# Kernel tuning notes

Hardware: AMD Instinct MI355X
Metric: run time of the kernel (lower is better)

Reference implementation:

```python
import jax, jax.numpy as jnp
import numpy as np
import math
from jax import lax


def _conv(x, w, b=None):
    # NCHW conv, stride 1, SAME padding (matches k=3,p=1 and k=1,p=0)
    y = lax.conv_general_dilated(x, w, (1, 1), 'SAME',
                                 dimension_numbers=('NCHW', 'OIHW', 'NCHW'))
    if b is not None:
        y = y + b[None, :, None, None]
    return y


def _bn(x):
    # BatchNorm2d(affine=False) in training mode: batch statistics, eps=1e-5
    m = x.mean(axis=(0, 2, 3), keepdims=True)
    v = x.var(axis=(0, 2, 3), keepdims=True)
    return (x - m) * lax.rsqrt(v + 1e-5)


def _basic(x, w):
    # BasicLayer: Conv -> BN(affine=False) -> ReLU
    return jax.nn.relu(_bn(_conv(x, w)))


def _grid_sample(img, grid):
    # torch F.grid_sample, mode='bilinear', align_corners=False, zero padding
    # img: (B,C,H,W), grid: (B,Hg,Wg,2) in [-1,1] (x,y)
    B, C, H, W = img.shape
    x = (grid[..., 0] + 1.0) * (W * 0.5) - 0.5
    y = (grid[..., 1] + 1.0) * (H * 0.5) - 0.5
    x0 = jnp.floor(x)
    y0 = jnp.floor(y)
    wx = x - x0
    wy = y - y0
    x0i = x0.astype(jnp.int32)
    y0i = y0.astype(jnp.int32)

    def samp(im, yi, xi):
        valid = ((xi >= 0) & (xi < W) & (yi >= 0) & (yi < H)).astype(im.dtype)
        v = im[:, jnp.clip(yi, 0, H - 1), jnp.clip(xi, 0, W - 1)]  # (C,Hg,Wg)
        return v * valid[None]

    def per_b(im, y0i, x0i, wx, wy):
        v00 = samp(im, y0i, x0i)
        v01 = samp(im, y0i, x0i + 1)
        v10 = samp(im, y0i + 1, x0i)
        v11 = samp(im, y0i + 1, x0i + 1)
        return (v00 * (1 - wx) * (1 - wy) + v01 * wx * (1 - wy)
                + v10 * (1 - wx) * wy + v11 * wx * wy)

    return jax.vmap(per_b)(img, y0i, x0i, wx, wy)


def _pos_grid(H, W, dtype):
    # meshgrid(indexing='xy'), stacked (x,y), reshaped row-major over (H,W)
    xs = jnp.linspace(-1 + 1.0 / W, 1 - 1.0 / W, W, dtype=dtype)
    ys = jnp.linspace(-1 + 1.0 / H, 1 - 1.0 / H, H, dtype=dtype)
    gx, gy = jnp.meshgrid(xs, ys, indexing='xy')  # (H,W)
    return jnp.stack([gx, gy], axis=-1).reshape(H * W, 2)


def setup_inputs() -> dict:
    key = jax.random.key(0)
    ks = jax.random.split(key, 16)
    B, Cc, Hc, Wc = 4, 64, 64, 64
    Cf, Hf, Wf = 24, 128, 128

    def w(k, shape):
        fan_in = shape[1] * shape[2] * shape[3]
        return jax.random.normal(k, shape, jnp.float32) / np.sqrt(fan_in).astype(np.float32)

    return {
        'feats0_c': jax.random.normal(ks[0], (B, Cc, Hc, Wc), jnp.float32),
        'feats1_c': jax.random.normal(ks[1], (B, Cc, Hc, Wc), jnp.float32),
        'feats0_f': jax.random.normal(ks[2], (B, Cf, Hf, Wf), jnp.float32),
        'feats1_f': jax.random.normal(ks[3], (B, Cf, Hf, Wf), jnp.float32),
        'cw1': w(ks[4], (256, 130, 3, 3)),
        'cw2': w(ks[5], (256, 256, 3, 3)),
        'cw3': w(ks[6], (256, 256, 3, 3)),
        'cw4': w(ks[7], (256, 256, 3, 3)),
        'cw5': w(ks[8], (3, 256, 1, 1)),
        'cb5': jax.random.normal(ks[9], (3,), jnp.float32) * 0.01,
        'fw1': w(ks[10], (64, 50, 3, 3)),
        'fw2': w(ks[11], (64, 64, 3, 3)),
        'fw3': w(ks[12], (64, 64, 3, 3)),
        'fw4': w(ks[13], (64, 64, 3, 3)),
        'fw5': w(ks[14], (3, 64, 1, 1)),
        'fb5': jax.random.normal(ks[15], (3,), jnp.float32) * 0.01,
    }


def reference(feats0_c, feats1_c, feats0_f, feats1_f,
              cw1, cw2, cw3, cw4, cw5, cb5,
              fw1, fw2, fw3, fw4, fw5, fb5):
    B, C, Hc, Wc = feats0_c.shape
    # corr_volume: einsum('bci,bcj->bji') -> (B, HW_1, Hc, Wc) over feat0 positions
    corr = jnp.einsum('bchw,bcj->bjhw', feats0_c,
                      feats1_c.reshape(B, C, Hc * Wc)) / math.sqrt(C)
    # pos_embed: softmax over feat1 positions, expected grid position
    P = jax.nn.softmax(corr, axis=1)
    g = _pos_grid(Hc, Wc, corr.dtype)  # (HW, 2)
    coarse_warp = jnp.einsum('bjhw,jd->bdhw', P, g)  # (B,2,Hc,Wc)
    coarse_matches0 = jnp.concatenate(
        [coarse_warp, jnp.zeros_like(coarse_warp[:, -1:])], axis=1)  # (B,3,Hc,Wc)

    warped1c = _grid_sample(feats1_c,
                            jnp.moveaxis(coarse_matches0, 1, -1)[..., :2])
    x = jnp.concatenate([feats0_c, warped1c, coarse_warp], axis=1)  # 130 ch
    for w_ in (cw1, cw2, cw3, cw4):
        x = _basic(x, w_)
    coarse_matches = coarse_matches0 + _conv(x, cw5, cb5)

    Hf, Wf = feats0_f.shape[-2:]
    up = jax.image.resize(coarse_matches, (B, 3, Hf, Wf), method='bilinear')
    up_d = lax.stop_gradient(up)  # torch .detach()
    warped1f = _grid_sample(feats1_f, jnp.moveaxis(up_d, 1, -1)[..., :2])
    y = jnp.concatenate([feats0_f, warped1f, up_d[:, :2]], axis=1)  # 50 ch
    for w_ in (fw1, fw2, fw3, fw4):
        y = _basic(y, w_)
    fine_matches = up_d + _conv(y, fw5, fb5)

    # corresps[8]['flow'/'certainty'] and corresps[4]['flow'/'certainty']
    return coarse_matches, fine_matches
```

## Files before the change

kernel.cpp:

```cpp
#include <hip/hip_runtime.h>
#include <hip/hip_bf16.h>

using bf16 = __hip_bfloat16;
typedef unsigned short ushort_t;
typedef __attribute__((ext_vector_type(8))) short v8s;
typedef __attribute__((ext_vector_type(4))) float v4f;

__device__ __forceinline__ float bfbits2f(unsigned u) {
    return __uint_as_float(u << 16);
}
__device__ __forceinline__ ushort_t f2bfbits(float f) {
    unsigned x = __float_as_uint(f);
    return (ushort_t)((x + 0x7fffu + ((x >> 16) & 1u)) >> 16);
}
__device__ __forceinline__ float ldin(const void* p, size_t i, int f32) {
    return f32 ? ((const float*)p)[i] : bfbits2f(((const ushort_t*)p)[i]);
}
__device__ __forceinline__ void stout(void* p, size_t i, float v, int f32) {
    if (f32) ((float*)p)[i] = v;
    else     ((ushort_t*)p)[i] = f2bfbits(v);
}

#define B_   4
#define CC   64
#define HC   64
#define WC   64
#define JC   4096
#define CF   24
#define HF   128
#define WF   128
#define JF   16384
#define OUT0_ELEMS (B_ * 3 * JC)

__global__ void dtype_probe_kernel(const ushort_t* __restrict__ x,
                                   int* __restrict__ flag)
{
    __shared__ int cnt;
    if (threadIdx.x == 0) cnt = 0;
    __syncthreads();
    int c = 0;
    for (int i = threadIdx.x; i < 8192; i += 256) {
        const unsigned e = (x[i] >> 7) & 0xFF;
        if (e >= 0x89) ++c;
    }
    atomicAdd(&cnt, c);
    __syncthreads();
    if (threadIdx.x == 0) *flag = (cnt > 64) ? 1 : 0;
}

__global__ void repack_w_kernel(const void* __restrict__ w, ushort_t* __restrict__ wp,
                                int CO, int CIreal, int CIP, const int* __restrict__ dflag)
{
    const int f32 = *dflag;
    const int idx = blockIdx.x * 256 + threadIdx.x;
    const int total = 9 * CO * CIP;
    if (idx >= total) return;
    const int k = idx / (CO * CIP);
    const int rem = idx - k * (CO * CIP);
    const int co = rem / CIP;
    const int cip = rem - co * CIP;
    float v = 0.f;
    if (cip < CIreal) v = ldin(w, ((size_t)co * CIreal + cip) * 9 + k, f32);
    wp[((size_t)k * CO + co) * CIP + cip] = f2bfbits(v);
}

__global__ void repack_wfrag_kernel(const void* __restrict__ w, ushort_t* __restrict__ wfrag,
                                    int CIreal, int nch, const int* __restrict__ dflag)
{
    const int f32 = *dflag;
    const int idx = blockIdx.x * 256 + threadIdx.x;
    const int total = 8 * 9 * 2 * 2 * nch * 64;
    if (idx >= total) return;
    const int ln = idx & 63;
    int t = idx >> 6;
    const int ch = t % nch; t /= nch;
    const int pl = t & 1; t >>= 1;
    const int nt = t & 1; t >>= 1;
    const int k = t % 9;
    const int cog = t / 9;
    const int co = cog * 32 + nt * 16 + (ln & 15);
    const int cib = ch * 32 + (ln >> 4) * 8;
    ushort_t vals[8];
#pragma unroll
    for (int e = 0; e < 8; ++e) {
        const int ci = cib + e;
        float v = 0.f;
        if (ci < CIreal) v = ldin(w, ((size_t)co * CIreal + ci) * 9 + k, f32);
        const ushort_t h = f2bfbits(v);
        vals[e] = pl ? f2bfbits(v - bfbits2f(h)) : h;
    }
    uint4 o;
    o.x = (unsigned)vals[0] | ((unsigned)vals[1] << 16);
    o.y = (unsigned)vals[2] | ((unsigned)vals[3] << 16);
    o.z = (unsigned)vals[4] | ((unsigned)vals[5] << 16);
    o.w = (unsigned)vals[6] | ((unsigned)vals[7] << 16);
    *(uint4*)&wfrag[(size_t)idx * 8] = o;
}

__global__ __launch_bounds__(256) void split_transpose_kernel(
    const void* __restrict__ src, ushort_t* __restrict__ hi,
    ushort_t* __restrict__ lo, const int* __restrict__ dflag)
{
    const int f32 = *dflag;
    __shared__ float t[64][65];
    const int blk = blockIdx.x;
    const int b = blk >> 6;
    const int px0 = (blk & 63) * 64;
    const int tid = threadIdx.x;
    const int px = tid & 63;
    for (int i = 0; i < 16; ++i) {
        const int c = (tid >> 6) + 4 * i;
        t[px][c] = ldin(src, ((size_t)b * 64 + c) * 4096 + px0 + px, f32);
    }
    __syncthreads();
    for (int it = 0; it < 2; ++it) {
        const int p = tid + it * 256;
        const int opx = p >> 3, chk = (p & 7) * 8;
        unsigned hh[4], ll[4];
#pragma unroll
        for (int e = 0; e < 4; ++e) {
            const float v0 = t[opx][chk + 2 * e];
            const float v1 = t[opx][chk + 2 * e + 1];
            const ushort_t h0 = f2bfbits(v0);
            const ushort_t h1 = f2bfbits(v1);
            hh[e] = (unsigned)h0 | ((unsigned)h1 << 16);
            ll[e] = (unsigned)f2bfbits(v0 - bfbits2f(h0))
                  | ((unsigned)f2bfbits(v1 - bfbits2f(h1)) << 16);
        }
        const size_t obase = ((size_t)b * 4096 + px0 + opx) * 64 + chk;
        *(uint4*)&hi[obase] = make_uint4(hh[0], hh[1], hh[2], hh[3]);
        *(uint4*)&lo[obase] = make_uint4(ll[0], ll[1], ll[2], ll[3]);
    }
}

#define KCH 128
__global__ __launch_bounds__(256) void corr_mfma_kernel(
    const ushort_t* __restrict__ qhi, const ushort_t* __restrict__ qlo,
    const ushort_t* __restrict__ khi, const ushort_t* __restrict__ klo,
    float* __restrict__ part)
{
    __shared__ ushort_t kbh[KCH * 72];
    __shared__ ushort_t kbl[KCH * 72];
    __shared__ float red[4][64][3];
    const int h = blockIdx.x, b = blockIdx.y, sl = blockIdx.z;
    const int tid = threadIdx.x;
    const int wv = tid >> 6, ln = tid & 63;
    const int lm = ln & 15, quad = ln >> 4, q8 = quad * 8;

    v8s qf[4][2][2];
#pragma unroll
    for (int mt = 0; mt < 4; ++mt)
#pragma unroll
        for (int kc = 0; kc < 2; ++kc) {
            const size_t qoff = ((size_t)b * 4096 + h * 64 + mt * 16 + lm) * 64 + kc * 32 + q8;
            qf[mt][kc][0] = *(const v8s*)&qhi[qoff];
            qf[mt][kc][1] = *(const v8s*)&qlo[qoff];
        }

    float P[4][4][3];
#pragma unroll
    for (int mt = 0; mt < 4; ++mt)
#pragma unroll
        for (int i = 0; i < 4; ++i)
            P[mt][i][0] = P[mt][i][1] = P[mt][i][2] = 0.f;

    const size_t kbase = (size_t)b * 4096 * 64;
    for (int c = 0; c < 1024 / KCH; ++c) {
        const int j0 = sl * 1024 + c * KCH;
        __syncthreads();
        for (int p = tid; p < 2048; p += 256) {
            const int pl = p >> 10;
            const int r = p & 1023;
            const int key = r >> 3, chk = (r & 7) * 8;
            const ushort_t* gsrc = pl ? klo : khi;
            const uint4 v = *(const uint4*)&gsrc[kbase + (size_t)(j0 + key) * 64 + chk];
            ushort_t* dst = pl ? kbl : kbh;
            *(uint4*)&dst[key * 72 + chk] = v;
        }
        __syncthreads();

#pragma unroll
        for (int nt = 0; nt < 2; ++nt) {
            const int kb = wv * 32 + nt * 16;
            const int j = j0 + kb + lm;
            const float gx = (float)((j & 63) * 2 + 1) * (1.f / 64.f) - 1.f;
            const float gy = (float)((j >> 6) * 2 + 1) * (1.f / 64.f) - 1.f;
            const v8s bh0 = *(const v8s*)&kbh[(kb + lm) * 72 + q8];
            const v8s bh1 = *(const v8s*)&kbh[(kb + lm) * 72 + 32 + q8];
            const v8s bl0 = *(const v8s*)&kbl[(kb + lm) * 72 + q8];
            const v8s bl1 = *(const v8s*)&kbl[(kb + lm) * 72 + 32 + q8];
#pragma unroll
            for (int mt = 0; mt < 4; ++mt) {
                v4f acc = (v4f)(0.f);
                acc = __builtin_amdgcn_mfma_f32_16x16x32_bf16(qf[mt][0][0], bl0, acc, 0, 0, 0);
                acc = __builtin_amdgcn_mfma_f32_16x16x32_bf16(qf[mt][0][1], bh0, acc, 0, 0, 0);
                acc = __builtin_amdgcn_mfma_f32_16x16x32_bf16(qf[mt][0][0], bh0, acc, 0, 0, 0);
                acc = __builtin_amdgcn_mfma_f32_16x16x32_bf16(qf[mt][1][0], bl1, acc, 0, 0, 0);
                acc = __builtin_amdgcn_mfma_f32_16x16x32_bf16(qf[mt][1][1], bh1, acc, 0, 0, 0);
                acc = __builtin_amdgcn_mfma_f32_16x16x32_bf16(qf[mt][1][0], bh1, acc, 0, 0, 0);
#pragma unroll
                for (int i = 0; i < 4; ++i) {
                    const float p_ = __expf(acc[i] * 0.125f);
                    P[mt][i][0] += p_;
                    P[mt][i][1] += p_ * gx;
                    P[mt][i][2] += p_ * gy;
                }
            }
        }
    }

#pragma unroll
    for (int mt = 0; mt < 4; ++mt)
#pragma unroll
        for (int i = 0; i < 4; ++i)
#pragma unroll
            for (int d = 0; d < 3; ++d) {
                float v = P[mt][i][d];
                v += __shfl_xor(v, 1);
                v += __shfl_xor(v, 2);
                v += __shfl_xor(v, 4);
                v += __shfl_xor(v, 8);
                P[mt][i][d] = v;
            }
    if (lm == 0) {
#pragma unroll
        for (int mt = 0; mt < 4; ++mt)
#pragma unroll
            for (int i = 0; i < 4; ++i) {
                const int q = mt * 16 + quad * 4 + i;
                red[wv][q][0] = P[mt][i][0];
                red[wv][q][1] = P[mt][i][1];
                red[wv][q][2] = P[mt][i][2];
            }
    }
    __syncthreads();
    if (tid < 64) {
        const int q = tid;
        float l = 0.f, ax = 0.f, ay = 0.f;
        for (int w = 0; w < 4; ++w) {
            l += red[w][q][0]; ax += red[w][q][1]; ay += red[w][q][2];
        }
        const size_t base = (((size_t)sl * B_ + b) * 4096 + h * 64 + q) * 4;
        part[base] = l; part[base + 1] = ax; part[base + 2] = ay;
    }
}

__global__ __launch_bounds__(256) void corr_reduce_kernel(
    const float* __restrict__ part, float* __restrict__ cm0)
{
    const int idx = blockIdx.x * 256 + threadIdx.x;
    const int b = idx >> 12, hq = idx & 4095;
    float l = 0.f, ax = 0.f, ay = 0.f;
    for (int s = 0; s < 4; ++s) {
        const size_t base = (((size_t)s * B_ + b) * 4096 + hq) * 4;
        l += part[base]; ax += part[base + 1]; ay += part[base + 2];
    }
    const float inv = 1.f / l;
    const size_t o = (size_t)b * 3 * JC + hq;
    cm0[o]          = ax * inv;
    cm0[o + JC]     = ay * inv;
    cm0[o + 2 * JC] = 0.f;
}

__global__ __launch_bounds__(256) void coarse_concat_split(
    const void* __restrict__ f0c, const void* __restrict__ f1c,
    const float* __restrict__ cm0, ushort_t* __restrict__ hiP,
    ushort_t* __restrict__ loP, const int* __restrict__ dflag)
{
    const int f32 = *dflag;
    const int idx = blockIdx.x * 256 + threadIdx.x;
    const int b = idx >> 12, hw = idx & (JC - 1);
    const size_t ib = (size_t)b * CC * JC;
    ushort_t* oh = hiP + (size_t)idx * 160;
    ushort_t* ol = loP + (size_t)idx * 160;

#pragma unroll 4
    for (int c = 0; c < CC; ++c) {
        const float v = ldin(f0c, ib + (size_t)c * JC + hw, f32);
        const ushort_t h = f2bfbits(v);
        oh[c] = h; ol[c] = f2bfbits(v - bfbits2f(h));
    }

    const float gx = cm0[((size_t)b * 3 + 0) * JC + hw];
    const float gy = cm0[((size_t)b * 3 + 1) * JC + hw];
    const float x = (gx + 1.f) * 32.f - 0.5f;
    const float y = (gy + 1.f) * 32.f - 0.5f;
    const float x0f = floorf(x), y0f = floorf(y);
    const float wx = x - x0f, wy = y - y0f;
    const int x0 = (int)x0f, y0 = (int)y0f;
    const int x1 = x0 + 1, y1 = y0 + 1;
    const float vx0 = (x0 >= 0 && x0 < WC) ? 1.f : 0.f;
    const float vx1 = (x1 >= 0 && x1 < WC) ? 1.f : 0.f;
    const float vy0 = (y0 >= 0 && y0 < HC) ? 1.f : 0.f;
    const float vy1 = (y1 >= 0 && y1 < HC) ? 1.f : 0.f;
    const int cx0 = min(max(x0, 0), WC - 1), cx1 = min(max(x1, 0), WC - 1);
    const int cy0 = min(max(y0, 0), HC - 1), cy1 = min(max(y1, 0), HC - 1);
    const float w00 = (1.f - wx) * (1.f - wy) * vx0 * vy0;
    const float w01 = wx * (1.f - wy) * vx1 * vy0;
    const float w10 = (1.f - wx) * wy * vx0 * vy1;
    const float w11 = wx * wy * vx1 * vy1;
    const int i00 = cy0 * WC + cx0, i01 = cy0 * WC + cx1;
    const int i10 = cy1 * WC + cx0, i11 = cy1 * WC + cx1;

#pragma unroll 4
    for (int c = 0; c < CC; ++c) {
        const size_t pb = ib + (size_t)c * JC;
        const float v = w00 * ldin(f1c, pb + i00, f32) + w01 * ldin(f1c, pb + i01, f32)
                      + w10 * ldin(f1c, pb + i10, f32) + w11 * ldin(f1c, pb + i11, f32);
        const ushort_t h = f2bfbits(v);
        oh[64 + c] = h; ol[64 + c] = f2bfbits(v - bfbits2f(h));
    }
    {
        const ushort_t h = f2bfbits(gx);
        oh[128] = h; ol[128] = f2bfbits(gx - bfbits2f(h));
    }
    {
        const ushort_t h = f2bfbits(gy);
        oh[129] = h; ol[129] = f2bfbits(gy - bfbits2f(h));
    }
    for (int c = 130; c < 160; ++c) { oh[c] = 0; ol[c] = 0; }
}

__global__ __launch_bounds__(256) void bnrelu_split_kernel(
    const float* __restrict__ x, const float2* __restrict__ st,
    ushort_t* __restrict__ hiP, ushort_t* __restrict__ loP)
{
    const int idx = blockIdx.x * 256 + threadIdx.x;
    const int px = idx >> 5;
    const int c8 = (idx & 31) << 3;
    const float4 v0 = *(const float4*)&x[(size_t)px * 256 + c8];
    const float4 v1 = *(const float4*)&x[(size_t)px * 256 + c8 + 4];
    const float vv[8] = {v0.x, v0.y, v0.z, v0.w, v1.x, v1.y, v1.z, v1.w};
    ushort_t hh[8], ll[8];
#pragma unroll
    for (int e = 0; e < 8; ++e) {
        const float2 s = st[c8 + e];
        const float f = fmaxf((vv[e] - s.x) * s.y, 0.f);
        const ushort_t h = f2bfbits(f);
        hh[e] = h; ll[e] = f2bfbits(f - bfbits2f(h));
    }
    uint4 oh, ol;
    oh.x = (unsigned)hh[0] | ((unsigned)hh[1] << 16);
    oh.y = (unsigned)hh[2] | ((unsigned)hh[3] << 16);
    oh.z = (unsigned)hh[4] | ((unsigned)hh[5] << 16);
    oh.w = (unsigned)hh[6] | ((unsigned)hh[7] << 16);
    ol.x = (unsigned)ll[0] | ((unsigned)ll[1] << 16);
    ol.y = (unsigned)ll[2] | ((unsigned)ll[3] << 16);
    ol.z = (unsigned)ll[4] | ((unsigned)ll[5] << 16);
    ol.w = (unsigned)ll[6] | ((unsigned)ll[7] << 16);
    *(uint4*)&hiP[(size_t)px * 256 + c8] = oh;
    *(uint4*)&loP[(size_t)px * 256 + c8] = ol;
}

__global__ __launch_bounds__(256, 3) void conv3x3_wsplit(
    const ushort_t* __restrict__ hiP, const ushort_t* __restrict__ loP,
    const ushort_t* __restrict__ wfrag,
    float* __restrict__ out, float* __restrict__ chsum,
    int CIP, int CO, int H, int W, int tilesX)
{
    __shared__ ushort_t actH[18 * 18 * 36];
    __shared__ ushort_t actL[18 * 18 * 36];
    __shared__ float smS[4][2][16], smQ[4][2][16];

    const int nch = CIP >> 5;
    const int tid = threadIdx.x;
    const int tile = blockIdx.x;
    const int b = blockIdx.y;
    const int cog = blockIdx.z;
    const int ty = (tile / tilesX) * 16;
    const int tx = (tile % tilesX) * 16;
    const int wv = tid >> 6;
    const int ln = tid & 63;
    const int lm = ln & 15;
    const int q8 = (ln >> 4) * 8;

    v4f acc[4][2];
#pragma unroll
    for (int i = 0; i < 4; ++i)
#pragma unroll
        for (int j = 0; j < 2; ++j) acc[i][j] = (v4f)(0.f);

    for (int ch = 0; ch < nch; ++ch) {
        const int ci0 = ch << 5;
        __syncthreads();
        for (int p = tid; p < 2592; p += 256) {
            const int pl = (p >= 1296) ? 1 : 0;
            const int r = p - pl * 1296;
            const int yy = r / 72;
            const int rem = r - yy * 72;
            const int xx = rem >> 2;
            const int cs = (rem & 3) << 3;
            const int gy = ty + yy - 1, gx = tx + xx - 1;
            uint4 val = make_uint4(0u, 0u, 0u, 0u);
            if (gy >= 0 && gy < H && gx >= 0 && gx < W) {
                const ushort_t* src = pl ? loP : hiP;
                val = *(const uint4*)&src[(((size_t)(b * H + gy)) * W + gx) * CIP + ci0 + cs];
            }
            ushort_t* dst = pl ? actL : actH;
            *(uint4*)&dst[(yy * 18 + xx) * 36 + cs] = val;
        }
        __syncthreads();

#pragma unroll
        for (int dx = 0; dx < 3; ++dx) {
            v8s ah[6], al[6];
#pragma unroll
            for (int rr = 0; rr < 6; ++rr) {
                const int aoff = ((wv * 4 + rr) * 18 + lm + dx) * 36 + q8;
                ah[rr] = *(const v8s*)&actH[aoff];
                al[rr] = *(const v8s*)&actL[aoff];
            }
#pragma unroll
            for (int dy = 0; dy < 3; ++dy) {
                const int k = dy * 3 + dx;
                const size_t fb = (((size_t)(cog * 9 + k) * 4) * nch + ch) * 64 + ln;
                const size_t step = (size_t)nch * 64;
                const v8s bh0 = *(const v8s*)&wfrag[fb * 8];
                const v8s bl0 = *(const v8s*)&wfrag[(fb + step) * 8];
                const v8s bh1 = *(const v8s*)&wfrag[(fb + 2 * step) * 8];
                const v8s bl1 = *(const v8s*)&wfrag[(fb + 3 * step) * 8];
#pragma unroll
                for (int mt = 0; mt < 4; ++mt) {
                    const v8s a_h = ah[mt + dy];
                    const v8s a_l = al[mt + dy];
                    acc[mt][0] = __builtin_amdgcn_mfma_f32_16x16x32_bf16(a_h, bl0, acc[mt][0], 0, 0, 0);
                    acc[mt][0] = __builtin_amdgcn_mfma_f32_16x16x32_bf16(a_l, bh0, acc[mt][0], 0, 0, 0);
                    acc[mt][0] = __builtin_amdgcn_mfma_f32_16x16x32_bf16(a_h, bh0, acc[mt][0], 0, 0, 0);
                    acc[mt][1] = __builtin_amdgcn_mfma_f32_16x16x32_bf16(a_h, bl1, acc[mt][1], 0, 0, 0);
                    acc[mt][1] = __builtin_amdgcn_mfma_f32_16x16x32_bf16(a_l, bh1, acc[mt][1], 0, 0, 0);
                    acc[mt][1] = __builtin_amdgcn_mfma_f32_16x16x32_bf16(a_h, bh1, acc[mt][1], 0, 0, 0);
                }
            }
        }
    }

#pragma unroll
    for (int mt = 0; mt < 4; ++mt) {
        const int y = ty + wv * 4 + mt;
#pragma unroll
        for (int nt = 0; nt < 2; ++nt) {
            const int co = cog * 32 + nt * 16 + lm;
#pragma unroll
            for (int i = 0; i < 4; ++i) {
                const int x = tx + ((ln >> 4) << 2) + i;
                out[(((size_t)(b * H + y)) * W + x) * CO + co] = acc[mt][nt][i];
            }
        }
    }

    float s0 = 0.f, s1 = 0.f, q0 = 0.f, q1 = 0.f;
#pragma unroll
    for (int mt = 0; mt < 4; ++mt)
#pragma unroll
        for (int i = 0; i < 4; ++i) {
            float v = acc[mt][0][i]; s0 += v; q0 += v * v;
            v = acc[mt][1][i]; s1 += v; q1 += v * v;
        }
    s0 += __shfl_xor(s0, 16); s0 += __shfl_xor(s0, 32);
    s1 += __shfl_xor(s1, 16); s1 += __shfl_xor(s1, 32);
    q0 += __shfl_xor(q0, 16); q0 += __shfl_xor(q0, 32);
    q1 += __shfl_xor(q1, 16); q1 += __shfl_xor(q1, 32);
    __syncthreads();
    if (ln < 16) {
        smS[wv][0][ln] = s0; smS[wv][1][ln] = s1;
        smQ[wv][0][ln] = q0; smQ[wv][1][ln] = q1;
    }
    __syncthreads();
    if (tid < 32) {
        const int nt = tid >> 4, l2 = tid & 15;
        float S = 0.f, Q = 0.f;
        for (int w = 0; w < 4; ++w) { S += smS[w][nt][l2]; Q += smQ[w][nt][l2]; }
        const int co = cog * 32 + nt * 16 + l2;
        atomicAdd(&chsum[2 * co], S);
        atomicAdd(&chsum[2 * co + 1], Q);
    }
}

template <bool BN>
__global__ __launch_bounds__(256) void conv3x3_mfma(
    const ushort_t* __restrict__ in,
    const ushort_t* __restrict__ wp,
    const float2* __restrict__ stats,
    ushort_t* __restrict__ out, float* __restrict__ chsum,
    int CI, int CO, int H, int W, int tilesX)
{
    __shared__ ushort_t act[18 * 18 * 40];
    __shared__ ushort_t wbuf[9 * 32 * 40];
    __shared__ float2 st[256];
    __shared__ float smS[4][2][16], smQ[4][2][16];

    const int tid = threadIdx.x;
    const int tile = blockIdx.x;
    const int b = blockIdx.y;
    const int cog = blockIdx.z;
    const int ty = (tile / tilesX) * 16;
    const int tx = (tile % tilesX) * 16;
    const int wv = tid >> 6;
    const int ln = tid & 63;
    const int lm = ln & 15;
    const int q8 = (ln >> 4) * 8;

    if (BN) for (int c = tid; c < CI; c += 256) st[c] = stats[c];

    v4f acc[4][2];
#pragma unroll
    for (int i = 0; i < 4; ++i)
#pragma unroll
        for (int j = 0; j < 2; ++j) acc[i][j] = (v4f)(0.f);

    const int nChunks = CI >> 5;
    for (int ch = 0; ch < nChunks; ++ch) {
        const int ci0 = ch << 5;
        __syncthreads();
        for (int p = tid; p < 1296; p += 256) {
            const int yy = p / 72;
            const int rem = p - yy * 72;
            const int xx = rem >> 2;
            const int cs = (rem & 3) << 3;
            const int gy = ty + yy - 1, gx = tx + xx - 1;
            uint4 val = make_uint4(0u, 0u, 0u, 0u);
            if (gy >= 0 && gy < H && gx >= 0 && gx < W) {
                const ushort_t* gp = in + (((size_t)(b * H + gy)) * W + gx) * CI + ci0 + cs;
                val = *(const uint4*)gp;
                if (BN) {
                    unsigned u[4] = {val.x, val.y, val.z, val.w};
                    unsigned o[4];
#pragma unroll
                    for (int e = 0; e < 4; ++e) {
                        float lo = bfbits2f(u[e] & 0xffffu);
                        float hi = bfbits2f(u[e] >> 16);
                        const float2 s0 = st[ci0 + cs + 2 * e];
                        const float2 s1 = st[ci0 + cs + 2 * e + 1];
                        lo = fmaxf((lo - s0.x) * s0.y, 0.f);
                        hi = fmaxf((hi - s1.x) * s1.y, 0.f);
                        o[e] = (unsigned)f2bfbits(lo) | ((unsigned)f2bfbits(hi) << 16);
                    }
                    val = make_uint4(o[0], o[1], o[2], o[3]);
                }
            }
            *(uint4*)&act[(yy * 18 + xx) * 40 + cs] = val;
        }
        for (int p = tid; p < 1152; p += 256) {
            const int k = p / 128;
            const int rem = p - k * 128;
            const int co = rem >> 2;
            const int cs = (rem & 3) << 3;
            const ushort_t* gp = wp + ((size_t)k * CO + cog * 32 + co) * CI + ci0 + cs;
            *(uint4*)&wbuf[(k * 32 + co) * 40 + cs] = *(const uint4*)gp;
        }
        __syncthreads();

#pragma unroll
        for (int dx = 0; dx < 3; ++dx) {
            v8s af[6];
#pragma unroll
            for (int rr = 0; rr < 6; ++rr)
                af[rr] = *(const v8s*)&act[((wv * 4 + rr) * 18 + lm + dx) * 40 + q8];
#pragma unroll
            for (int dy = 0; dy < 3; ++dy) {
                const int k = dy * 3 + dx;
                const v8s bf0 = *(const v8s*)&wbuf[(k * 32 + lm) * 40 + q8];
                const v8s bf1 = *(const v8s*)&wbuf[(k * 32 + 16 + lm) * 40 + q8];
#pragma unroll
                for (int mt = 0; mt < 4; ++mt) {
                    acc[mt][0] = __builtin_amdgcn_mfma_f32_16x16x32_bf16(af[mt + dy], bf0, acc[mt][0], 0, 0, 0);
                    acc[mt][1] = __builtin_amdgcn_mfma_f32_16x16x32_bf16(af[mt + dy], bf1, acc[mt][1], 0, 0, 0);
                }
            }
        }
    }

#pragma unroll
    for (int mt = 0; mt < 4; ++mt) {
        const int y = ty + wv * 4 + mt;
#pragma unroll
        for (int nt = 0; nt < 2; ++nt) {
            const int co = cog * 32 + nt * 16 + lm;
#pragma unroll
            for (int i = 0; i < 4; ++i) {
                const int x = tx + ((ln >> 4) << 2) + i;
                out[(((size_t)(b * H + y)) * W + x) * CO + co] = f2bfbits(acc[mt][nt][i]);
            }
        }
    }

    float s0 = 0.f, s1 = 0.f, q0 = 0.f, q1 = 0.f;
#pragma unroll
    for (int mt = 0; mt < 4; ++mt)
#pragma unroll
        for (int i = 0; i < 4; ++i) {
            float v = acc[mt][0][i]; s0 += v; q0 += v * v;
            v = acc[mt][1][i]; s1 += v; q1 += v * v;
        }
    s0 += __shfl_xor(s0, 16); s0 += __shfl_xor(s0, 32);
    s1 += __shfl_xor(s1, 16); s1 += __shfl_xor(s1, 32);
    q0 += __shfl_xor(q0, 16); q0 += __shfl_xor(q0, 32);
    q1 += __shfl_xor(q1, 16); q1 += __shfl_xor(q1, 32);
    __syncthreads();
    if (ln < 16) {
        smS[wv][0][ln] = s0; smS[wv][1][ln] = s1;
        smQ[wv][0][ln] = q0; smQ[wv][1][ln] = q1;
    }
    __syncthreads();
    if (tid < 32) {
        const int nt = tid >> 4, l2 = tid & 15;
        float S = 0.f, Q = 0.f;
        for (int w = 0; w < 4; ++w) { S += smS[w][nt][l2]; Q += smQ[w][nt][l2]; }
        const int co = cog * 32 + nt * 16 + l2;
        atomicAdd(&chsum[2 * co], S);
        atomicAdd(&chsum[2 * co + 1], Q);
    }
}

__global__ void stats_finalize_kernel(const float* __restrict__ chsum,
                                      float2* __restrict__ st, int C, float inv_n)
{
    const int c = threadIdx.x;
    if (c >= C) return;
    const float mean = chsum[2 * c] * inv_n;
    const float var = chsum[2 * c + 1] * inv_n - mean * mean;
    st[c] = make_float2(mean, 1.0f / sqrtf(var + 1e-5f));
}

__global__ __launch_bounds__(256) void coarse_head_kernel(
    const float* __restrict__ A, const float2* __restrict__ stats,
    const void* __restrict__ w5, const void* __restrict__ b5,
    float* __restrict__ cm0, void* __restrict__ out,
    const int* __restrict__ dflag)
{
    const int f32 = *dflag;
    __shared__ float wl[3][256];
    __shared__ float bl[3];
    __shared__ float2 st[256];
    const int tid = threadIdx.x;
    for (int i = tid; i < 768; i += 256) wl[i >> 8][i & 255] = ldin(w5, i, f32);
    if (tid < 3) bl[tid] = ldin(b5, tid, f32);
    st[tid] = stats[tid];
    __syncthreads();

    const int idx = blockIdx.x * 256 + tid;
    const int b = idx >> 12, hw = idx & (JC - 1);
    float a0 = bl[0], a1 = bl[1], a2 = bl[2];
    const float* p = A + (size_t)idx * 256;
    for (int c = 0; c < 256; c += 4) {
        const float4 raw = *(const float4*)(p + c);
        const float rv[4] = {raw.x, raw.y, raw.z, raw.w};
#pragma unroll
        for (int e = 0; e < 4; ++e) {
            const int cc = c + e;
            const float v = fmaxf((rv[e] - st[cc].x) * st[cc].y, 0.f);
            a0 += v * wl[0][cc]; a1 += v * wl[1][cc]; a2 += v * wl[2][cc];
        }
    }
    const size_t base = (size_t)b * 3 * JC + hw;
    const float c0 = cm0[base] + a0;
    const float c1 = cm0[base + JC] + a1;
    const float c2 = cm0[base + 2 * JC] + a2;
    cm0[base] = c0; cm0[base + JC] = c1; cm0[base + 2 * JC] = c2;
    stout(out, base, c0, f32);
    stout(out, base + JC, c1, f32);
    stout(out, base + 2 * JC, c2, f32);
}

__global__ __launch_bounds__(256) void upsample_kernel(
    const float* __restrict__ cm, float* __restrict__ up)
{
    const int idx = blockIdx.x * 256 + threadIdx.x;
    const int ox = idx & 127, oy = (idx >> 7) & 127, bc = idx >> 14;
    const float sx = ox * 0.5f - 0.25f;
    const float sy = oy * 0.5f - 0.25f;
    const int x0 = (int)floorf(sx), y0 = (int)floorf(sy);
    const float fx = sx - x0, fy = sy - y0;
    const int cx0 = max(x0, 0), cx1 = min(x0 + 1, WC - 1);
    const int cy0 = max(y0, 0), cy1 = min(y0 + 1, HC - 1);
    const float* p = cm + (size_t)bc * JC;
    const float v = (1.f - fy) * ((1.f - fx) * p[cy0 * WC + cx0] + fx * p[cy0 * WC + cx1])
                  + fy * ((1.f - fx) * p[cy1 * WC + cx0] + fx * p[cy1 * WC + cx1]);
    up[idx] = v;
}

__global__ __launch_bounds__(256) void fine_concat_nhwc(
    const void* __restrict__ f0f, const void* __restrict__ f1f,
    const float* __restrict__ up, ushort_t* __restrict__ A,
    const int* __restrict__ dflag)
{
    const int f32 = *dflag;
    const int idx = blockIdx.x * 256 + threadIdx.x;
    const int b = idx >> 14, hw = idx & (JF - 1);
    const size_t ib = (size_t)b * CF * JF;
    ushort_t* o = A + (size_t)idx * 64;

    for (int c = 0; c < CF; ++c)
        o[c] = f2bfbits(ldin(f0f, ib + (size_t)c * JF + hw, f32));

    const size_t ub = (size_t)b * 3 * JF + hw;
    const float gx = up[ub], gy = up[ub + JF];
    const float x = (gx + 1.f) * 64.f - 0.5f;
    const float y = (gy + 1.f) * 64.f - 0.5f;
    const float x0f = floorf(x), y0f = floorf(y);
    const float wx = x - x0f, wy = y - y0f;
    const int x0 = (int)x0f, y0 = (int)y0f;
    const int x1 = x0 + 1, y1 = y0 + 1;
    const float vx0 = (x0 >= 0 && x0 < WF) ? 1.f : 0.f;
    const float vx1 = (x1 >= 0 && x1 < WF) ? 1.f : 0.f;
    const float vy0 = (y0 >= 0 && y0 < HF) ? 1.f : 0.f;
    const float vy1 = (y1 >= 0 && y1 < HF) ? 1.f : 0.f;
    const int cx0 = min(max(x0, 0), WF - 1), cx1 = min(max(x1, 0), WF - 1);
    const int cy0 = min(max(y0, 0), HF - 1), cy1 = min(max(y1, 0), HF - 1);
    const float w00 = (1.f - wx) * (1.f - wy) * vx0 * vy0;
    const float w01 = wx * (1.f - wy) * vx1 * vy0;
    const float w10 = (1.f - wx) * wy * vx0 * vy1;
    const float w11 = wx * wy * vx1 * vy1;
    const int i00 = cy0 * WF + cx0, i01 = cy0 * WF + cx1;
    const int i10 = cy1 * WF + cx0, i11 = cy1 * WF + cx1;

    for (int c = 0; c < CF; ++c) {
        const size_t pb = ib + (size_t)c * JF;
        const float v = w00 * ldin(f1f, pb + i00, f32) + w01 * ldin(f1f, pb + i01, f32)
                      + w10 * ldin(f1f, pb + i10, f32) + w11 * ldin(f1f, pb + i11, f32);
        o[24 + c] = f2bfbits(v);
    }
    o[48] = f2bfbits(gx);
    o[49] = f2bfbits(gy);
    for (int c = 50; c < 64; ++c) o[c] = 0;
}

__global__ __launch_bounds__(256) void fine_head_kernel(
    const ushort_t* __restrict__ A, const float2* __restrict__ stats,
    const void* __restrict__ w5, const void* __restrict__ b5,
    const float* __restrict__ up, void* __restrict__ out,
    const int* __restrict__ dflag)
{
    const int f32 = *dflag;
    __shared__ float wl[3][64];
    __shared__ float bl[3];
    __shared__ float2 st[64];
    const int tid = threadIdx.x;
    if (tid < 192) wl[tid >> 6][tid & 63] = ldin(w5, tid, f32);
    if (tid < 3) bl[tid] = ldin(b5, tid, f32);
    if (tid < 64) st[tid] = stats[tid];
    __syncthreads();

    const int idx = blockIdx.x * 256 + tid;
    const int b = idx >> 14, hw = idx & (JF - 1);
    float a0 = bl[0], a1 = bl[1], a2 = bl[2];
    const ushort_t* p = A + (size_t)idx * 64;
    for (int c = 0; c < 64; c += 8) {
        const uint4 raw = *(const uint4*)(p + c);
        const unsigned u[4] = {raw.x, raw.y, raw.z, raw.w};
#pragma unroll
        for (int e = 0; e < 4; ++e) {
            const int c0 = c + 2 * e, c1 = c0 + 1;
            float lo = bfbits2f(u[e] & 0xffffu);
            float hi = bfbits2f(u[e] >> 16);
            lo = fmaxf((lo - st[c0].x) * st[c0].y, 0.f);
            hi = fmaxf((hi - st[c1].x) * st[c1].y, 0.f);
            a0 += lo * wl[0][c0] + hi * wl[0][c1];
            a1 += lo * wl[1][c0] + hi * wl[1][c1];
            a2 += lo * wl[2][c0] + hi * wl[2][c1];
        }
    }
    const size_t base = (size_t)b * 3 * JF + hw;
    stout(out, OUT0_ELEMS + base,          up[base] + a0, f32);
    stout(out, OUT0_ELEMS + base + JF,     up[base + JF] + a1, f32);
    stout(out, OUT0_ELEMS + base + 2 * JF, up[base + 2 * JF] + a2, f32);
}

extern "C" void kernel_launch(void* const* d_in, const int* in_sizes, int n_in,
                              void* d_out, int out_size, void* d_ws, size_t ws_size,
                              hipStream_t stream)
{
    const void* f0c = d_in[0];
    const void* f1c = d_in[1];
    const void* f0f = d_in[2];
    const void* f1f = d_in[3];
    const void* cw1 = d_in[4];
    const void* cw2 = d_in[5];
    const void* cw3 = d_in[6];
    const void* cw4 = d_in[7];
    const void* cw5 = d_in[8];
    const void* cb5 = d_in[9];
    const void* fw1 = d_in[10];
    const void* fw2 = d_in[11];
    const void* fw3 = d_in[12];
    const void* fw4 = d_in[13];
    const void* fw5 = d_in[14];
    const void* fb5 = d_in[15];

    char* wsb = (char*)d_ws;
    float* bufA    = (float*)wsb;
    float* bufB    = (float*)(wsb + 16777216);
    float* cm0     = (float*)(wsb + 33554432);
    float* up      = (float*)(wsb + 33751040);
    float* chsum   = (float*)(wsb + 34537472);
    float2* st_g   = (float2*)(wsb + 34668544);
    int* dflag     = (int*)(wsb + 34670592);
    ushort_t* fwp  = (ushort_t*)(wsb + 34670656);
    ushort_t* fw1p = fwp;
    ushort_t* fw2p = fwp + 36864;
    ushort_t* fw3p = fwp + 73728;
    ushort_t* fw4p = fwp + 110592;
    ushort_t* wfrag = (ushort_t*)(wsb + 34965568);

    ushort_t* hiP = (ushort_t*)bufA;
    ushort_t* loP = (ushort_t*)(wsb + 8388608);

    ushort_t* qhi = (ushort_t*)bufA;
    ushort_t* qlo = qhi + 1048576;
    ushort_t* khi = qlo + 1048576;
    ushort_t* klo = khi + 1048576;
    float* cpart = (float*)bufB;

    ushort_t* fF1 = (ushort_t*)bufB;
    ushort_t* fF2 = (ushort_t*)bufA;

    dtype_probe_kernel<<<1, 256, 0, stream>>>((const ushort_t*)f0c, dflag);

    repack_w_kernel<<<(9 * 64 * 64 + 255) / 256, 256, 0, stream>>>(fw1, fw1p, 64, 50, 64, dflag);
    repack_w_kernel<<<(9 * 64 * 64 + 255) / 256, 256, 0, stream>>>(fw2, fw2p, 64, 64, 64, dflag);
    repack_w_kernel<<<(9 * 64 * 64 + 255) / 256, 256, 0, stream>>>(fw3, fw3p, 64, 64, 64, dflag);
    repack_w_kernel<<<(9 * 64 * 64 + 255) / 256, 256, 0, stream>>>(fw4, fw4p, 64, 64, 64, dflag);

    split_transpose_kernel<<<dim3(B_ * 64), 256, 0, stream>>>(f0c, qhi, qlo, dflag);
    split_transpose_kernel<<<dim3(B_ * 64), 256, 0, stream>>>(f1c, khi, klo, dflag);
    corr_mfma_kernel<<<dim3(HC, B_, 4), 256, 0, stream>>>(qhi, qlo, khi, klo, cpart);
    corr_reduce_kernel<<<dim3(B_ * JC / 256), 256, 0, stream>>>(cpart, cm0);

    coarse_concat_split<<<dim3(B_ * JC / 256), 256, 0, stream>>>(f0c, f1c, cm0, hiP, loP, dflag);

    const dim3 cgrid(16, B_, 8);
    repack_wfrag_kernel<<<(8 * 9 * 2 * 2 * 5 * 64 + 255) / 256, 256, 0, stream>>>(cw1, wfrag, 130, 5, dflag);
    hipMemsetAsync(chsum, 0, 2048, stream);
    conv3x3_wsplit<<<cgrid, 256, 0, stream>>>(hiP, loP, wfrag, bufB, chsum, 160, 256, HC, WC, 4);
    stats_finalize_kernel<<<1, 256, 0, stream>>>(chsum, st_g, 256, 1.f / 16384.f);

    bnrelu_split_kernel<<<B_ * JC * 32 / 256, 256, 0, stream>>>(bufB, st_g, hiP, loP);
    repack_wfrag_kernel<<<(8 * 9 * 2 * 2 * 8 * 64 + 255) / 256, 256, 0, stream>>>(cw2, wfrag, 256, 8, dflag);
    hipMemsetAsync(chsum, 0, 2048, stream);
    conv3x3_wsplit<<<cgrid, 256, 0, stream>>>(hiP, loP, wfrag, bufB, chsum, 256, 256, HC, WC, 4);
    stats_finalize_kernel<<<1, 256, 0, stream>>>(chsum, st_g, 256, 1.f / 16384.f);

    bnrelu_split_kernel<<<B_ * JC * 32 / 256, 256, 0, stream>>>(bufB, st_g, hiP, loP);
    repack_wfrag_kernel<<<(8 * 9 * 2 * 2 * 8 * 64 + 255) / 256, 256, 0, stream>>>(cw3, wfrag, 256, 8, dflag);
    hipMemsetAsync(chsum, 0, 2048, stream);
    conv3x3_wsplit<<<cgrid, 256, 0, stream>>>(hiP, loP, wfrag, bufB, chsum, 256, 256, HC, WC, 4);
    stats_finalize_kernel<<<1, 256, 0, stream>>>(chsum, st_g, 256, 1.f / 16384.f);

    bnrelu_split_kernel<<<B_ * JC * 32 / 256, 256, 0, stream>>>(bufB, st_g, hiP, loP);
    repack_wfrag_kernel<<<(8 * 9 * 2 * 2 * 8 * 64 + 255) / 256, 256, 0, stream>>>(cw4, wfrag, 256, 8, dflag);
    hipMemsetAsync(chsum, 0, 2048, stream);
    conv3x3_wsplit<<<cgrid, 256, 0, stream>>>(hiP, loP, wfrag, bufB, chsum, 256, 256, HC, WC, 4);
    stats_finalize_kernel<<<1, 256, 0, stream>>>(chsum, st_g, 256, 1.f / 16384.f);

    coarse_head_kernel<<<dim3(B_ * JC / 256), 256, 0, stream>>>(bufB, st_g, cw5, cb5, cm0, d_out, dflag);

    upsample_kernel<<<dim3(B_ * 3 * JF / 256), 256, 0, stream>>>(cm0, up);

    fine_concat_nhwc<<<dim3(B_ * JF / 256), 256, 0, stream>>>(f0f, f1f, up, fF1, dflag);

    const dim3 fgrid(64, B_, 2);
    hipMemsetAsync(chsum, 0, 512, stream);
    conv3x3_mfma<false><<<fgrid, 256, 0, stream>>>(fF1, fw1p, nullptr, fF2, chsum, 64, 64, HF, WF, 8);
    stats_finalize_kernel<<<1, 256, 0, stream>>>(chsum, st_g, 64, 1.f / 65536.f);
    hipMemsetAsync(chsum, 0, 512, stream);
    conv3x3_mfma<true><<<fgrid, 256, 0, stream>>>(fF2, fw2p, st_g, fF1, chsum, 64, 64, HF, WF, 8);
    stats_finalize_kernel<<<1, 256, 0, stream>>>(chsum, st_g, 64, 1.f / 65536.f);
    hipMemsetAsync(chsum, 0, 512, stream);
    conv3x3_mfma<true><<<fgrid, 256, 0, stream>>>(fF1, fw3p, st_g, fF2, chsum, 64, 64, HF, WF, 8);
    stats_finalize_kernel<<<1, 256, 0, stream>>>(chsum, st_g, 64, 1.f / 65536.f);
    hipMemsetAsync(chsum, 0, 512, stream);
    conv3x3_mfma<true><<<fgrid, 256, 0, stream>>>(fF2, fw4p, st_g, fF1, chsum, 64, 64, HF, WF, 8);
    stats_finalize_kernel<<<1, 256, 0, stream>>>(chsum, st_g, 64, 1.f / 65536.f);

    fine_head_kernel<<<dim3(B_ * JF / 256), 256, 0, stream>>>(fF1, st_g, fw5, fb5, up, d_out, dflag);
}
```

Measured before the change: 805.6 us.

## Halve conv3x3 tile height and double-buffer weight fragments in registers

```diff
diff --git a/kernel.cpp b/kernel.cpp
--- a/kernel.cpp
+++ b/kernel.cpp
@@ -352,14 +352,16 @@
     *(uint4*)&loP[(size_t)px * 256 + c8] = ol;
 }
 
+struct WFrags { v8s bh0[3], bl0[3], bh1[3], bl1[3]; };
+
 __global__ __launch_bounds__(256, 3) void conv3x3_wsplit(
     const ushort_t* __restrict__ hiP, const ushort_t* __restrict__ loP,
     const ushort_t* __restrict__ wfrag,
     float* __restrict__ out, float* __restrict__ chsum,
     int CIP, int CO, int H, int W, int tilesX)
 {
-    __shared__ ushort_t actH[18 * 18 * 36];
-    __shared__ ushort_t actL[18 * 18 * 36];
+    __shared__ ushort_t actH[10 * 18 * 36];
+    __shared__ ushort_t actL[10 * 18 * 36];
     __shared__ float smS[4][2][16], smQ[4][2][16];
 
     const int nch = CIP >> 5;
@@ -367,25 +369,57 @@
     const int tile = blockIdx.x;
     const int b = blockIdx.y;
     const int cog = blockIdx.z;
-    const int ty = (tile / tilesX) * 16;
+    const int ty = (tile / tilesX) * 8;
     const int tx = (tile % tilesX) * 16;
     const int wv = tid >> 6;
     const int ln = tid & 63;
     const int lm = ln & 15;
     const int q8 = (ln >> 4) * 8;
-
-    v4f acc[4][2];
-#pragma unroll
-    for (int i = 0; i < 4; ++i)
+    const size_t step = (size_t)nch * 64;
+
+    v4f acc[2][2];
+#pragma unroll
+    for (int i = 0; i < 2; ++i)
 #pragma unroll
         for (int j = 0; j < 2; ++j) acc[i][j] = (v4f)(0.f);
+
+    WFrags FA, FB;
+
+    auto loadF = [&](WFrags& F, int ch, int dx) {
+#pragma unroll
+        for (int dy = 0; dy < 3; ++dy) {
+            const int k = dy * 3 + dx;
+            const size_t fb = (((size_t)(cog * 9 + k) * 4) * nch + ch) * 64 + ln;
+            F.bh0[dy] = *(const v8s*)&wfrag[fb * 8];
+            F.bl0[dy] = *(const v8s*)&wfrag[(fb + step) * 8];
+            F.bh1[dy] = *(const v8s*)&wfrag[(fb + 2 * step) * 8];
+            F.bl1[dy] = *(const v8s*)&wfrag[(fb + 3 * step) * 8];
+        }
+    };
+    auto computeF = [&](const WFrags& F, int dx) {
+#pragma unroll
+        for (int dy = 0; dy < 3; ++dy) {
+#pragma unroll
+            for (int mt = 0; mt < 2; ++mt) {
+                const int aoff = ((wv * 2 + mt + dy) * 18 + lm + dx) * 36 + q8;
+                const v8s a_h = *(const v8s*)&actH[aoff];
+                const v8s a_l = *(const v8s*)&actL[aoff];
+                acc[mt][0] = __builtin_amdgcn_mfma_f32_16x16x32_bf16(a_h, F.bl0[dy], acc[mt][0], 0, 0, 0);
+                acc[mt][0] = __builtin_amdgcn_mfma_f32_16x16x32_bf16(a_l, F.bh0[dy], acc[mt][0], 0, 0, 0);
+                acc[mt][0] = __builtin_amdgcn_mfma_f32_16x16x32_bf16(a_h, F.bh0[dy], acc[mt][0], 0, 0, 0);
+                acc[mt][1] = __builtin_amdgcn_mfma_f32_16x16x32_bf16(a_h, F.bl1[dy], acc[mt][1], 0, 0, 0);
+                acc[mt][1] = __builtin_amdgcn_mfma_f32_16x16x32_bf16(a_l, F.bh1[dy], acc[mt][1], 0, 0, 0);
+                acc[mt][1] = __builtin_amdgcn_mfma_f32_16x16x32_bf16(a_h, F.bh1[dy], acc[mt][1], 0, 0, 0);
+            }
+        }
+    };
 
     for (int ch = 0; ch < nch; ++ch) {
         const int ci0 = ch << 5;
         __syncthreads();
-        for (int p = tid; p < 2592; p += 256) {
-            const int pl = (p >= 1296) ? 1 : 0;
-            const int r = p - pl * 1296;
+        for (int p = tid; p < 1440; p += 256) {
+            const int pl = (p >= 720) ? 1 : 0;
+            const int r = p - pl * 720;
             const int yy = r / 72;
             const int rem = r - yy * 72;
             const int xx = rem >> 2;
@@ -401,42 +435,17 @@
         }
         __syncthreads();
 
-#pragma unroll
-        for (int dx = 0; dx < 3; ++dx) {
-            v8s ah[6], al[6];
-#pragma unroll
-            for (int rr = 0; rr < 6; ++rr) {
-                const int aoff = ((wv * 4 + rr) * 18 + lm + dx) * 36 + q8;
-                ah[rr] = *(const v8s*)&actH[aoff];
-                al[rr] = *(const v8s*)&actL[aoff];
-            }
-#pragma unroll
-            for (int dy = 0; dy < 3; ++dy) {
-                const int k = dy * 3 + dx;
-                const size_t fb = (((size_t)(cog * 9 + k) * 4) * nch + ch) * 64 + ln;
-                const size_t step = (size_t)nch * 64;
-                const v8s bh0 = *(const v8s*)&wfrag[fb * 8];
-                const v8s bl0 = *(const v8s*)&wfrag[(fb + step) * 8];
-                const v8s bh1 = *(const v8s*)&wfrag[(fb + 2 * step) * 8];
-                const v8s bl1 = *(const v8s*)&wfrag[(fb + 3 * step) * 8];
-#pragma unroll
-                for (int mt = 0; mt < 4; ++mt) {
-                    const v8s a_h = ah[mt + dy];
-                    const v8s a_l = al[mt + dy];
-                    acc[mt][0] = __builtin_amdgcn_mfma_f32_16x16x32_bf16(a_h, bl0, acc[mt][0], 0, 0, 0);
-                    acc[mt][0] = __builtin_amdgcn_mfma_f32_16x16x32_bf16(a_l, bh0, acc[mt][0], 0, 0, 0);
-                    acc[mt][0] = __builtin_amdgcn_mfma_f32_16x16x32_bf16(a_h, bh0, acc[mt][0], 0, 0, 0);
-                    acc[mt][1] = __builtin_amdgcn_mfma_f32_16x16x32_bf16(a_h, bl1, acc[mt][1], 0, 0, 0);
-                    acc[mt][1] = __builtin_amdgcn_mfma_f32_16x16x32_bf16(a_l, bh1, acc[mt][1], 0, 0, 0);
-                    acc[mt][1] = __builtin_amdgcn_mfma_f32_16x16x32_bf16(a_h, bh1, acc[mt][1], 0, 0, 0);
-                }
-            }
-        }
-    }
-
-#pragma unroll
-    for (int mt = 0; mt < 4; ++mt) {
-        const int y = ty + wv * 4 + mt;
+        loadF(FA, ch, 0);
+        loadF(FB, ch, 1);
+        computeF(FA, 0);
+        loadF(FA, ch, 2);
+        computeF(FB, 1);
+        computeF(FA, 2);
+    }
+
+#pragma unroll
+    for (int mt = 0; mt < 2; ++mt) {
+        const int y = ty + wv * 2 + mt;
 #pragma unroll
         for (int nt = 0; nt < 2; ++nt) {
             const int co = cog * 32 + nt * 16 + lm;
@@ -450,7 +459,7 @@
 
     float s0 = 0.f, s1 = 0.f, q0 = 0.f, q1 = 0.f;
 #pragma unroll
-    for (int mt = 0; mt < 4; ++mt)
+    for (int mt = 0; mt < 2; ++mt)
 #pragma unroll
         for (int i = 0; i < 4; ++i) {
             float v = acc[mt][0][i]; s0 += v; q0 += v * v;
@@ -828,7 +837,7 @@
 
     coarse_concat_split<<<dim3(B_ * JC / 256), 256, 0, stream>>>(f0c, f1c, cm0, hiP, loP, dflag);
 
-    const dim3 cgrid(16, B_, 8);
+    const dim3 cgrid(32, B_, 8);
     repack_wfrag_kernel<<<(8 * 9 * 2 * 2 * 5 * 64 + 255) / 256, 256, 0, stream>>>(cw1, wfrag, 130, 5, dflag);
     hipMemsetAsync(chsum, 0, 2048, stream);
     conv3x3_wsplit<<<cgrid, 256, 0, stream>>>(hiP, loP, wfrag, bufB, chsum, 160, 256, HC, WC, 4);
```

Result: no change. 798.4 us (-0.9%).

## Retile coarse split-bf16 conv to 8-row tiles covering two output-channel groups

Applied to the files above, without the earlier changes.

```diff
diff --git a/kernel.cpp b/kernel.cpp
--- a/kernel.cpp
+++ b/kernel.cpp
@@ -358,34 +358,37 @@
     float* __restrict__ out, float* __restrict__ chsum,
     int CIP, int CO, int H, int W, int tilesX)
 {
-    __shared__ ushort_t actH[18 * 18 * 36];
-    __shared__ ushort_t actL[18 * 18 * 36];
-    __shared__ float smS[4][2][16], smQ[4][2][16];
+    __shared__ ushort_t actH[10 * 18 * 36];
+    __shared__ ushort_t actL[10 * 18 * 36];
+    __shared__ float smS[4][2][2][16], smQ[4][2][2][16];
 
     const int nch = CIP >> 5;
     const int tid = threadIdx.x;
     const int tile = blockIdx.x;
     const int b = blockIdx.y;
-    const int cog = blockIdx.z;
-    const int ty = (tile / tilesX) * 16;
+    const int cog2 = blockIdx.z;
+    const int ty = (tile / tilesX) * 8;
     const int tx = (tile % tilesX) * 16;
     const int wv = tid >> 6;
     const int ln = tid & 63;
     const int lm = ln & 15;
     const int q8 = (ln >> 4) * 8;
-
-    v4f acc[4][2];
-#pragma unroll
-    for (int i = 0; i < 4; ++i)
-#pragma unroll
-        for (int j = 0; j < 2; ++j) acc[i][j] = (v4f)(0.f);
+    const size_t step = (size_t)nch * 64;
+
+    v4f acc[2][2][2];
+#pragma unroll
+    for (int g = 0; g < 2; ++g)
+#pragma unroll
+        for (int i = 0; i < 2; ++i)
+#pragma unroll
+            for (int j = 0; j < 2; ++j) acc[g][i][j] = (v4f)(0.f);
 
     for (int ch = 0; ch < nch; ++ch) {
         const int ci0 = ch << 5;
         __syncthreads();
-        for (int p = tid; p < 2592; p += 256) {
-            const int pl = (p >= 1296) ? 1 : 0;
-            const int r = p - pl * 1296;
+        for (int p = tid; p < 1440; p += 256) {
+            const int pl = (p >= 720) ? 1 : 0;
+            const int r = p - pl * 720;
             const int yy = r / 72;
             const int rem = r - yy * 72;
             const int xx = rem >> 2;
@@ -403,76 +406,92 @@
 
 #pragma unroll
         for (int dx = 0; dx < 3; ++dx) {
-            v8s ah[6], al[6];
-#pragma unroll
-            for (int rr = 0; rr < 6; ++rr) {
-                const int aoff = ((wv * 4 + rr) * 18 + lm + dx) * 36 + q8;
+            v8s ah[4], al[4];
+#pragma unroll
+            for (int rr = 0; rr < 4; ++rr) {
+                const int aoff = ((wv * 2 + rr) * 18 + lm + dx) * 36 + q8;
                 ah[rr] = *(const v8s*)&actH[aoff];
                 al[rr] = *(const v8s*)&actL[aoff];
             }
 #pragma unroll
-            for (int dy = 0; dy < 3; ++dy) {
-                const int k = dy * 3 + dx;
-                const size_t fb = (((size_t)(cog * 9 + k) * 4) * nch + ch) * 64 + ln;
-                const size_t step = (size_t)nch * 64;
-                const v8s bh0 = *(const v8s*)&wfrag[fb * 8];
-                const v8s bl0 = *(const v8s*)&wfrag[(fb + step) * 8];
-                const v8s bh1 = *(const v8s*)&wfrag[(fb + 2 * step) * 8];
-                const v8s bl1 = *(const v8s*)&wfrag[(fb + 3 * step) * 8];
-#pragma unroll
-                for (int mt = 0; mt < 4; ++mt) {
-                    const v8s a_h = ah[mt + dy];
-                    const v8s a_l = al[mt + dy];
-                    acc[mt][0] = __builtin_amdgcn_mfma_f32_16x16x32_bf16(a_h, bl0, acc[mt][0], 0, 0, 0);
-                    acc[mt][0] = __builtin_amdgcn_mfma_f32_16x16x32_bf16(a_l, bh0, acc[mt][0], 0, 0, 0);
-                    acc[mt][0] = __builtin_amdgcn_mfma_f32_16x16x32_bf16(a_h, bh0, acc[mt][0], 0, 0, 0);
-                    acc[mt][1] = __builtin_amdgcn_mfma_f32_16x16x32_bf16(a_h, bl1, acc[mt][1], 0, 0, 0);
-                    acc[mt][1] = __builtin_amdgcn_mfma_f32_16x16x32_bf16(a_l, bh1, acc[mt][1], 0, 0, 0);
-                    acc[mt][1] = __builtin_amdgcn_mfma_f32_16x16x32_bf16(a_h, bh1, acc[mt][1], 0, 0, 0);
+            for (int g = 0; g < 2; ++g) {
+                const int cog = cog2 * 2 + g;
+#pragma unroll
+                for (int dy = 0; dy < 3; ++dy) {
+                    const int k = dy * 3 + dx;
+                    const size_t fb = (((size_t)(cog * 9 + k) * 4) * nch + ch) * 64 + ln;
+                    const v8s bh0 = *(const v8s*)&wfrag[fb * 8];
+                    const v8s bl0 = *(const v8s*)&wfrag[(fb + step) * 8];
+                    const v8s bh1 = *(const v8s*)&wfrag[(fb + 2 * step) * 8];
+                    const v8s bl1 = *(const v8s*)&wfrag[(fb + 3 * step) * 8];
+#pragma unroll
+                    for (int mt = 0; mt < 2; ++mt) {
+                        const v8s a_h = ah[mt + dy];
+                        const v8s a_l = al[mt + dy];
+                        acc[g][mt][0] = __builtin_amdgcn_mfma_f32_16x16x32_bf16(a_h, bl0, acc[g][mt][0], 0, 0, 0);
+                        acc[g][mt][0] = __builtin_amdgcn_mfma_f32_16x16x32_bf16(a_l, bh0, acc[g][mt][0], 0, 0, 0);
+                        acc[g][mt][0] = __builtin_amdgcn_mfma_f32_16x16x32_bf16(a_h, bh0, acc[g][mt][0], 0, 0, 0);
+                        acc[g][mt][1] = __builtin_amdgcn_mfma_f32_16x16x32_bf16(a_h, bl1, acc[g][mt][1], 0, 0, 0);
+                        acc[g][mt][1] = __builtin_amdgcn_mfma_f32_16x16x32_bf16(a_l, bh1, acc[g][mt][1], 0, 0, 0);
+                        acc[g][mt][1] = __builtin_amdgcn_mfma_f32_16x16x32_bf16(a_h, bh1, acc[g][mt][1], 0, 0, 0);
+                    }
                 }
             }
         }
     }
 
 #pragma unroll
-    for (int mt = 0; mt < 4; ++mt) {
-        const int y = ty + wv * 4 + mt;
+    for (int g = 0; g < 2; ++g) {
+#pragma unroll
+        for (int mt = 0; mt < 2; ++mt) {
+            const int y = ty + wv * 2 + mt;
+#pragma unroll
+            for (int nt = 0; nt < 2; ++nt) {
+                const int co = (cog2 * 2 + g) * 32 + nt * 16 + lm;
+#pragma unroll
+                for (int i = 0; i < 4; ++i) {
+                    const int x = tx + ((ln >> 4) << 2) + i;
+                    out[(((size_t)(b * H + y)) * W + x) * CO + co] = acc[g][mt][nt][i];
+                }
+            }
+        }
+    }
+
+    float S[2][2], Q[2][2];
+#pragma unroll
+    for (int g = 0; g < 2; ++g)
 #pragma unroll
         for (int nt = 0; nt < 2; ++nt) {
-            const int co = cog * 32 + nt * 16 + lm;
-#pragma unroll
-            for (int i = 0; i < 4; ++i) {
-                const int x = tx + ((ln >> 4) << 2) + i;
-                out[(((size_t)(b * H + y)) * W + x) * CO + co] = acc[mt][nt][i];
-            }
-        }
-    }
-
-    float s0 = 0.f, s1 = 0.f, q0 = 0.f, q1 = 0.f;
-#pragma unroll
-    for (int mt = 0; mt < 4; ++mt)
-#pragma unroll
-        for (int i = 0; i < 4; ++i) {
-            float v = acc[mt][0][i]; s0 += v; q0 += v * v;
-            v = acc[mt][1][i]; s1 += v; q1 += v * v;
-        }
-    s0 += __shfl_xor(s0, 16); s0 += __shfl_xor(s0, 32);
-    s1 += __shfl_xor(s1, 16); s1 += __shfl_xor(s1, 32);
-    q0 += __shfl_xor(q0, 16); q0 += __shfl_xor(q0, 32);
-    q1 += __shfl_xor(q1, 16); q1 += __shfl_xor(q1, 32);
+            float s = 0.f, q = 0.f;
+#pragma unroll
+            for (int mt = 0; mt < 2; ++mt)
+#pragma unroll
+                for (int i = 0; i < 4; ++i) {
+                    const float v = acc[g][mt][nt][i];
+                    s += v; q += v * v;
+                }
+            s += __shfl_xor(s, 16); s += __shfl_xor(s, 32);
+            q += __shfl_xor(q, 16); q += __shfl_xor(q, 32);
+            S[g][nt] = s; Q[g][nt] = q;
+        }
     __syncthreads();
     if (ln < 16) {
-        smS[wv][0][ln] = s0; smS[wv][1][ln] = s1;
-        smQ[wv][0][ln] = q0; smQ[wv][1][ln] = q1;
-    }
-    __syncthreads();
-    if (tid < 32) {
-        const int nt = tid >> 4, l2 = tid & 15;
-        float S = 0.f, Q = 0.f;
-        for (int w = 0; w < 4; ++w) { S += smS[w][nt][l2]; Q += smQ[w][nt][l2]; }
-        const int co = cog * 32 + nt * 16 + l2;
-        atomicAdd(&chsum[2 * co], S);
-        atomicAdd(&chsum[2 * co + 1], Q);
+#pragma unroll
+        for (int g = 0; g < 2; ++g)
+#pragma unroll
+            for (int nt = 0; nt < 2; ++nt) {
+                smS[wv][g][nt][ln] = S[g][nt];
+                smQ[wv][g][nt][ln] = Q[g][nt];
+            }
+    }
+    __syncthreads();
+    if (tid < 64) {
+        const int g = tid >> 5, nt = (tid >> 4) & 1, l2 = tid & 15;
+        float Ssum = 0.f, Qsum = 0.f;
+        for (int w = 0; w < 4; ++w) { Ssum += smS[w][g][nt][l2]; Qsum += smQ[w][g][nt][l2]; }
+        const int co = (cog2 * 2 + g) * 32 + nt * 16 + l2;
+        atomicAdd(&chsum[2 * co], Ssum);
+        atomicAdd(&chsum[2 * co + 1], Qsum);
     }
 }
 
@@ -828,7 +847,7 @@
 
     coarse_concat_split<<<dim3(B_ * JC / 256), 256, 0, stream>>>(f0c, f1c, cm0, hiP, loP, dflag);
 
-    const dim3 cgrid(16, B_, 8);
+    const dim3 cgrid(32, B_, 4);
     repack_wfrag_kernel<<<(8 * 9 * 2 * 2 * 5 * 64 + 255) / 256, 256, 0, stream>>>(cw1, wfrag, 130, 5, dflag);
     hipMemsetAsync(chsum, 0, 2048, stream);
     conv3x3_wsplit<<<cgrid, 256, 0, stream>>>(hiP, loP, wfrag, bufB, chsum, 160, 256, HC, WC, 4);
```

Result: slower. 853.7 us (+6.0%).
